# Optimization experiments

Hardware: AMD Instinct MI355X
Metric: run time of the kernel (lower is better)

The kernel has to match this reference:

```python
import jax, jax.numpy as jnp
import numpy as np

H = 300
V = 19495
B = 64
TU = 50
TT = 64


def gru(x, h0, Wih, Whh, bih, bhh, lens=None):
    """PyTorch-equation GRU, batch_first. x:[B,T,H], h0:[B,H].
    If lens is given, emulates pack/pad: outputs are zero past len,
    hidden state stops updating past len (final h = state at last valid step)."""
    Bx, T, _ = x.shape
    xg = jnp.einsum('bth,gh->btg', x, Wih) + bih          # [B,T,3H]
    xg = jnp.transpose(xg, (1, 0, 2))                      # [T,B,3H]
    if lens is None:
        mask = jnp.ones((T, Bx, 1), x.dtype)
    else:
        mask = (jnp.arange(T)[:, None] < lens[None, :]).astype(x.dtype)[..., None]  # [T,B,1]

    def step(h, tm):
        xg_t, m = tm
        hg = h @ Whh.T + bhh
        xr, xz, xn = jnp.split(xg_t, 3, axis=-1)
        hr, hz, hn = jnp.split(hg, 3, axis=-1)
        r = jax.nn.sigmoid(xr + hr)
        z = jax.nn.sigmoid(xz + hz)
        n = jnp.tanh(xn + r * hn)
        h_new = (1.0 - z) * n + z * h
        h = m * h_new + (1.0 - m) * h
        return h, h_new * m

    h_last, outs = jax.lax.scan(step, h0, (xg, mask))
    return jnp.transpose(outs, (1, 0, 2)), h_last


def setup_inputs() -> dict:
    key = jax.random.key(0)
    ks = jax.random.split(key, 24)
    s = 0.05
    p = {}
    p['emb_table'] = jax.random.normal(ks[0], (V, H), jnp.float32) * s
    for i, name in enumerate(['enc', 'sess', 'dec']):
        p[name + '_Wih'] = jax.random.normal(ks[1 + 4 * i], (3 * H, H), jnp.float32) * s
        p[name + '_Whh'] = jax.random.normal(ks[2 + 4 * i], (3 * H, H), jnp.float32) * s
        p[name + '_bih'] = jax.random.normal(ks[3 + 4 * i], (3 * H,), jnp.float32) * s
        p[name + '_bhh'] = jax.random.normal(ks[4 + 4 * i], (3 * H,), jnp.float32) * s
    p['out_W'] = jax.random.normal(ks[13], (V, H), jnp.float32) * s
    p['out_b'] = jax.random.normal(ks[14], (V,), jnp.float32) * s
    p['u1_input'] = jax.random.randint(ks[15], (B, TU), 0, V, jnp.int32)
    p['u1_lens'] = jax.random.randint(ks[16], (B,), 1, TU + 1, jnp.int32)
    p['u2_input'] = jax.random.randint(ks[17], (B, TU), 0, V, jnp.int32)
    p['u2_lens'] = jax.random.randint(ks[18], (B,), 1, TU + 1, jnp.int32)
    p['target_input'] = jax.random.randint(ks[19], (B, TT), 0, V, jnp.int32)
    p['target_input_lens'] = jax.random.randint(ks[20], (B,), 1, TT + 1, jnp.int32)
    return p


def reference(emb_table, enc_Wih, enc_Whh, enc_bih, enc_bhh,
              sess_Wih, sess_Whh, sess_bih, sess_bhh,
              dec_Wih, dec_Whh, dec_bih, dec_bhh,
              out_W, out_b,
              u1_input, u1_lens, u2_input, u2_lens,
              target_input, target_input_lens):
    h0 = jnp.zeros((B, H), jnp.float32)
    # utterance encoders (shared GRU), pack/pad semantics via masking
    _, u1_h = gru(emb_table[u1_input], h0, enc_Wih, enc_Whh, enc_bih, enc_bhh, u1_lens)
    _, u2_h = gru(emb_table[u2_input], h0, enc_Wih, enc_Whh, enc_bih, enc_bhh, u2_lens)
    si = jnp.stack([u1_h, u2_h], axis=1)  # [B,2,H]
    _, sess_h = gru(si, h0, sess_Wih, sess_Whh, sess_bih, sess_bhh)
    # teacher-forced decoder over all target steps
    tgt_emb = emb_table[target_input]      # [B,TT,H]
    dec_outs, _ = gru(tgt_emb, sess_h, dec_Wih, dec_Whh, dec_bih, dec_bhh)
    logits = jnp.einsum('bth,vh->btv', dec_outs, out_W) + out_b  # [B,TT,V]
    return logits
```

## Files before the change

### kernel.cpp

```cpp
#include <hip/hip_runtime.h>
#include <hip/hip_bf16.h>


#define HDIM 300
#define H3   900
#define KP   320
#define NV   19495
#define NVP  19584
#define NB   64
#define TUL  50
#define TTL  64

typedef short short8 __attribute__((ext_vector_type(8)));
typedef float f32x4  __attribute__((ext_vector_type(4)));

__device__ inline unsigned short f32_to_bf16(float f) {
  unsigned int u = __float_as_uint(f);
  u = u + 0x7FFFu + ((u >> 16) & 1u);
  return (unsigned short)(u >> 16);
}

__global__ void convert_pad_kernel(const float* __restrict__ src, short* __restrict__ dst, int rows) {
  int total = rows * HDIM;
  for (int i = blockIdx.x * blockDim.x + threadIdx.x; i < total; i += gridDim.x * blockDim.x) {
    int r = i / HDIM, c = i - r * HDIM;
    dst[(long)r * KP + c] = (short)f32_to_bf16(src[i]);
  }
}

__global__ void convert_A_kernel(const float* __restrict__ hdec, short* __restrict__ dst) {
  int total = TTL * HDIM * NB;
  for (int i = blockIdx.x * blockDim.x + threadIdx.x; i < total; i += gridDim.x * blockDim.x) {
    int t = i / (HDIM * NB);
    int rem = i - t * (HDIM * NB);
    int j = rem / NB;
    int b = rem - j * NB;
    dst[(long)(b * TTL + t) * KP + j] = (short)f32_to_bf16(hdec[i]);
  }
}

#define GM_PROJ 0
#define GM_XGE  1
#define GM_XGD  2

template <int MODE>
__launch_bounds__(256)
__global__ void mfma_gemm_kernel(const short* __restrict__ A,
                                 const short* __restrict__ B,
                                 const float* __restrict__ bias,
                                 float* __restrict__ C,
                                 const int* __restrict__ idx1,
                                 const int* __restrict__ idx2) {
  __shared__ short Asm[128 * 40];
  __shared__ short Bsm[128 * 40];
  int tid = threadIdx.x;
  int lane = tid & 63, wid = tid >> 6;
  int wm = wid >> 1, wn = wid & 1;
  int m0 = blockIdx.y * 128, n0 = blockIdx.x * 128;

  f32x4 acc[4][4] = {};

  int lrow = tid >> 2, lq = tid & 3;
  long arow[2], brow[2];
#pragma unroll
  for (int h = 0; h < 2; ++h) {
    int m = m0 + lrow + h * 64;
    long rowbase;
    if (MODE == GM_PROJ) {
      rowbase = (long)m * KP;
    } else if (MODE == GM_XGD) {
      rowbase = (long)idx1[m] * KP;
    } else {
      int u = m / 3200;
      int rm = m - u * 3200;
      int b = rm / TUL;
      int t = rm - b * TUL;
      int iv = u ? idx2[b * TUL + t] : idx1[b * TUL + t];
      rowbase = (long)iv * KP;
    }
    arow[h] = rowbase + lq * 8;
    brow[h] = (long)(n0 + lrow + h * 64) * KP + lq * 8;
  }

  for (int k0 = 0; k0 < KP; k0 += 32) {
#pragma unroll
    for (int h = 0; h < 2; ++h) {
      *(short8*)&Asm[(lrow + h * 64) * 40 + lq * 8] = *(const short8*)&A[arow[h] + k0];
      *(short8*)&Bsm[(lrow + h * 64) * 40 + lq * 8] = *(const short8*)&B[brow[h] + k0];
    }
    __syncthreads();
    int rlo = lane & 15, khi = (lane >> 4) * 8;
    short8 af[4], bfv[4];
#pragma unroll
    for (int i = 0; i < 4; ++i) af[i]  = *(const short8*)&Asm[(wm * 64 + i * 16 + rlo) * 40 + khi];
#pragma unroll
    for (int i = 0; i < 4; ++i) bfv[i] = *(const short8*)&Bsm[(wn * 64 + i * 16 + rlo) * 40 + khi];
#pragma unroll
    for (int i = 0; i < 4; ++i)
#pragma unroll
      for (int j = 0; j < 4; ++j)
        acc[i][j] = __builtin_amdgcn_mfma_f32_16x16x32_bf16(af[i], bfv[j], acc[i][j], 0, 0, 0);
    __syncthreads();
  }

  int rhi = (lane >> 4) * 4, cl = lane & 15;
#pragma unroll
  for (int i = 0; i < 4; ++i)
#pragma unroll
    for (int j = 0; j < 4; ++j) {
      int mb = m0 + wm * 64 + i * 16 + rhi;
      int n = n0 + wn * 64 + j * 16 + cl;
#pragma unroll
      for (int r = 0; r < 4; ++r) {
        int m = mb + r;
        float v = acc[i][j][r];
        if (MODE == GM_PROJ) {
          if (n < NV) C[(long)m * NV + n] = v + bias[n];
        } else if (MODE == GM_XGD) {
          if (n < H3) {
            int b = m >> 6, t = m & 63;
            C[(long)t * (H3 * NB) + n * NB + b] = v + bias[n];
          }
        } else {
          if (n < H3) {
            int u = m / 3200;
            int rm = m - u * 3200;
            int b = rm / TUL;
            int t = rm - b * TUL;
            C[(long)t * (H3 * 128) + n * 128 + u * 64 + b] = v + bias[n];
          }
        }
      }
    }
}

template <int BW, bool CX>
__launch_bounds__(256)
__global__ void gru_step_kernel(const float* __restrict__ Whh, const float* __restrict__ bhh,
                                const float* __restrict__ xg,
                                const float* __restrict__ Wih, const float* __restrict__ bih,
                                const float* __restrict__ x, int xstride,
                                const float* __restrict__ hin, float* __restrict__ hout,
                                const int* __restrict__ len1, const int* __restrict__ len2, int t) {
  int gt = blockIdx.x * blockDim.x + threadIdx.x;
  if (gt >= HDIM * BW) return;
  int col = gt & (BW - 1);
  int j = gt / BW;

  float hr = bhh[j], hz = bhh[HDIM + j], hn = bhh[2 * HDIM + j];
  const float* wr = Whh + (long)j * HDIM;
  const float* wz = Whh + (long)(HDIM + j) * HDIM;
  const float* wn = Whh + (long)(2 * HDIM + j) * HDIM;
  float xr = 0.f, xz = 0.f, xn = 0.f;
  const float* vr = nullptr;
  const float* vz = nullptr;
  const float* vn = nullptr;
  if (CX) {
    xr = bih[j]; xz = bih[HDIM + j]; xn = bih[2 * HDIM + j];
    vr = Wih + (long)j * HDIM;
    vz = Wih + (long)(HDIM + j) * HDIM;
    vn = Wih + (long)(2 * HDIM + j) * HDIM;
  }

#pragma unroll 4
  for (int k = 0; k < HDIM; ++k) {
    float hv = hin[k * BW + col];
    hr = fmaf(wr[k], hv, hr);
    hz = fmaf(wz[k], hv, hz);
    hn = fmaf(wn[k], hv, hn);
    if (CX) {
      float xv = x[k * xstride + col];
      xr = fmaf(vr[k], xv, xr);
      xz = fmaf(vz[k], xv, xz);
      xn = fmaf(vn[k], xv, xn);
    }
  }
  if (!CX) {
    xr = xg[j * BW + col];
    xz = xg[(HDIM + j) * BW + col];
    xn = xg[(2 * HDIM + j) * BW + col];
  }
  float r = 1.f / (1.f + __expf(-(xr + hr)));
  float z = 1.f / (1.f + __expf(-(xz + hz)));
  float n = tanhf(xn + r * hn);
  float hprev = hin[j * BW + col];
  float hnew = (1.f - z) * n + z * hprev;
  if (len1 != nullptr) {
    int L = (col < 64) ? len1[col] : len2[col - 64];
    if (t >= L) hnew = hprev;
  }
  hout[j * BW + col] = hnew;
}

extern "C" void kernel_launch(void* const* d_in, const int* in_sizes, int n_in,
                              void* d_out, int out_size, void* d_ws, size_t ws_size,
                              hipStream_t stream) {
  const float* emb      = (const float*)d_in[0];
  const float* enc_Wih  = (const float*)d_in[1];
  const float* enc_Whh  = (const float*)d_in[2];
  const float* enc_bih  = (const float*)d_in[3];
  const float* enc_bhh  = (const float*)d_in[4];
  const float* sess_Wih = (const float*)d_in[5];
  const float* sess_Whh = (const float*)d_in[6];
  const float* sess_bih = (const float*)d_in[7];
  const float* sess_bhh = (const float*)d_in[8];
  const float* dec_Wih  = (const float*)d_in[9];
  const float* dec_Whh  = (const float*)d_in[10];
  const float* dec_bih  = (const float*)d_in[11];
  const float* dec_bhh  = (const float*)d_in[12];
  const float* out_W    = (const float*)d_in[13];
  const float* out_b    = (const float*)d_in[14];
  const int* u1_in      = (const int*)d_in[15];
  const int* u1_lens    = (const int*)d_in[16];
  const int* u2_in      = (const int*)d_in[17];
  const int* u2_lens    = (const int*)d_in[18];
  const int* tgt_in     = (const int*)d_in[19];
  float* out = (float*)d_out;

  char* w = (char*)d_ws;
  auto alloc = [&](size_t bytes) -> char* {
    char* p = w;
    w += (bytes + 255) & ~(size_t)255;
    return p;
  };
  short* emb_bf  = (short*)alloc((size_t)NV  * KP * 2);
  short* wie_bf  = (short*)alloc((size_t)1024 * KP * 2);
  short* wid_bf  = (short*)alloc((size_t)1024 * KP * 2);
  short* wout_bf = (short*)alloc((size_t)NVP * KP * 2);
  short* a_bf    = (short*)alloc((size_t)4096 * KP * 2);
  char* bf_end = w;
  float* h_enc0 = (float*)alloc((size_t)HDIM * 128 * 4);
  float* h_enc1 = (float*)alloc((size_t)HDIM * 128 * 4);
  float* h_s0   = (float*)alloc((size_t)HDIM * NB * 4);
  float* h_s1   = (float*)alloc((size_t)HDIM * NB * 4);
  char* h_end = w;
  float* xg_enc = (float*)alloc((size_t)TUL * H3 * 128 * 4);
  float* xg_dec = (float*)alloc((size_t)TTL * H3 * NB * 4);
  float* h_dec  = (float*)alloc((size_t)TTL * HDIM * NB * 4);

  hipMemsetAsync(emb_bf, 0, (size_t)(bf_end - (char*)emb_bf), stream);
  hipMemsetAsync(h_enc0, 0, (size_t)(h_end - (char*)h_enc0), stream);

  convert_pad_kernel<<<1024, 256, 0, stream>>>(emb, emb_bf, NV);
  convert_pad_kernel<<<64, 256, 0, stream>>>(enc_Wih, wie_bf, H3);
  convert_pad_kernel<<<64, 256, 0, stream>>>(dec_Wih, wid_bf, H3);
  convert_pad_kernel<<<1024, 256, 0, stream>>>(out_W, wout_bf, NV);

  {
    dim3 g(8, 50);
    mfma_gemm_kernel<GM_XGE><<<g, 256, 0, stream>>>(emb_bf, wie_bf, enc_bih, xg_enc, u1_in, u2_in);
  }
  {
    dim3 g(8, 32);
    mfma_gemm_kernel<GM_XGD><<<g, 256, 0, stream>>>(emb_bf, wid_bf, dec_bih, xg_dec, tgt_in, nullptr);
  }

  float* hb[2] = {h_enc0, h_enc1};
  for (int t = 0; t < TUL; ++t) {
    gru_step_kernel<128, false><<<150, 256, 0, stream>>>(
        enc_Whh, enc_bhh, xg_enc + (long)t * H3 * 128,
        nullptr, nullptr, nullptr, 0,
        hb[t & 1], hb[(t + 1) & 1], u1_lens, u2_lens, t);
  }
  float* encf = hb[0];

  float* sb[2] = {h_s0, h_s1};
  for (int t = 0; t < 2; ++t) {
    gru_step_kernel<64, true><<<75, 256, 0, stream>>>(
        sess_Whh, sess_bhh, nullptr,
        sess_Wih, sess_bih, encf + t * 64, 128,
        sb[t & 1], sb[(t + 1) & 1], nullptr, nullptr, t);
  }
  float* sessf = sb[0];

  for (int t = 0; t < TTL; ++t) {
    const float* hin = (t == 0) ? sessf : (h_dec + (long)(t - 1) * HDIM * NB);
    gru_step_kernel<64, false><<<75, 256, 0, stream>>>(
        dec_Whh, dec_bhh, xg_dec + (long)t * H3 * NB,
        nullptr, nullptr, nullptr, 0,
        hin, h_dec + (long)t * HDIM * NB, nullptr, nullptr, t);
  }

  convert_A_kernel<<<512, 256, 0, stream>>>(h_dec, a_bf);
  {
    dim3 g(153, 32);
    mfma_gemm_kernel<GM_PROJ><<<g, 256, 0, stream>>>(a_bf, wout_bf, out_b, out, nullptr, nullptr);
  }
}
```

Before: 3.518 ms.

## Fuse all GRU recurrences into one persistent MFMA kernel per batch slice

Replaces the 116 per-timestep fp32 GRU step launches and the separate conversion kernel with a single persistent kernel of 8 blocks. Each block owns 8 batch rows and keeps its hidden state in shared memory across the encoder, session and decoder phases. The recurrent matvecs run as bf16 MFMA, and the bf16 decoder outputs are written straight into the projection A matrix. This removes launch overhead and the global round trips of hidden state, but uses only 8 CUs and re-reads the recurrent weights from L2 every step. Rounding the recurrent weights and state to bf16 adds precision risk.

```diff
diff --git a/kernel.cpp b/kernel.cpp
--- a/kernel.cpp
+++ b/kernel.cpp
@@ -10,6 +10,8 @@
 #define NB   64
 #define TUL  50
 #define TTL  64
+#define HS   328
+#define HFS  301
 
 typedef short short8 __attribute__((ext_vector_type(8)));
 typedef float f32x4  __attribute__((ext_vector_type(4)));
@@ -25,17 +27,6 @@
   for (int i = blockIdx.x * blockDim.x + threadIdx.x; i < total; i += gridDim.x * blockDim.x) {
     int r = i / HDIM, c = i - r * HDIM;
     dst[(long)r * KP + c] = (short)f32_to_bf16(src[i]);
-  }
-}
-
-__global__ void convert_A_kernel(const float* __restrict__ hdec, short* __restrict__ dst) {
-  int total = TTL * HDIM * NB;
-  for (int i = blockIdx.x * blockDim.x + threadIdx.x; i < total; i += gridDim.x * blockDim.x) {
-    int t = i / (HDIM * NB);
-    int rem = i - t * (HDIM * NB);
-    int j = rem / NB;
-    int b = rem - j * NB;
-    dst[(long)(b * TTL + t) * KP + j] = (short)f32_to_bf16(hdec[i]);
   }
 }
 
@@ -134,62 +125,160 @@
     }
 }
 
-template <int BW, bool CX>
-__launch_bounds__(256)
-__global__ void gru_step_kernel(const float* __restrict__ Whh, const float* __restrict__ bhh,
-                                const float* __restrict__ xg,
-                                const float* __restrict__ Wih, const float* __restrict__ bih,
-                                const float* __restrict__ x, int xstride,
-                                const float* __restrict__ hin, float* __restrict__ hout,
-                                const int* __restrict__ len1, const int* __restrict__ len2, int t) {
-  int gt = blockIdx.x * blockDim.x + threadIdx.x;
-  if (gt >= HDIM * BW) return;
-  int col = gt & (BW - 1);
-  int j = gt / BW;
-
-  float hr = bhh[j], hz = bhh[HDIM + j], hn = bhh[2 * HDIM + j];
-  const float* wr = Whh + (long)j * HDIM;
-  const float* wz = Whh + (long)(HDIM + j) * HDIM;
-  const float* wn = Whh + (long)(2 * HDIM + j) * HDIM;
-  float xr = 0.f, xz = 0.f, xn = 0.f;
-  const float* vr = nullptr;
-  const float* vz = nullptr;
-  const float* vn = nullptr;
-  if (CX) {
-    xr = bih[j]; xz = bih[HDIM + j]; xn = bih[2 * HDIM + j];
-    vr = Wih + (long)j * HDIM;
-    vz = Wih + (long)(HDIM + j) * HDIM;
-    vn = Wih + (long)(2 * HDIM + j) * HDIM;
-  }
-
-#pragma unroll 4
-  for (int k = 0; k < HDIM; ++k) {
-    float hv = hin[k * BW + col];
-    hr = fmaf(wr[k], hv, hr);
-    hz = fmaf(wz[k], hv, hz);
-    hn = fmaf(wn[k], hv, hn);
-    if (CX) {
-      float xv = x[k * xstride + col];
-      xr = fmaf(vr[k], xv, xr);
-      xz = fmaf(vz[k], xv, xz);
-      xn = fmaf(vn[k], xv, xn);
-    }
-  }
-  if (!CX) {
-    xr = xg[j * BW + col];
-    xz = xg[(HDIM + j) * BW + col];
-    xn = xg[(2 * HDIM + j) * BW + col];
-  }
-  float r = 1.f / (1.f + __expf(-(xr + hr)));
-  float z = 1.f / (1.f + __expf(-(xz + hz)));
-  float n = tanhf(xn + r * hn);
-  float hprev = hin[j * BW + col];
-  float hnew = (1.f - z) * n + z * hprev;
-  if (len1 != nullptr) {
-    int L = (col < 64) ? len1[col] : len2[col - 64];
-    if (t >= L) hnew = hprev;
-  }
-  hout[j * BW + col] = hnew;
+__device__ __forceinline__ void run_chunks(const short* __restrict__ Wb,
+                                           const short8 (&af)[10],
+                                           f32x4 (&acc)[5][3],
+                                           int wv, int lane) {
+  int jc = lane & 15;
+  int kh = (lane >> 4) * 8;
+  short8 bb[3][10];
+  auto issue = [&](int c, short8 (&buf)[10]) {
+    int tw = c / 3, g = c - tw * 3;
+    const short* p = Wb + (long)(g * HDIM + (wv + 4 * tw) * 16 + jc) * KP + kh;
+#pragma unroll
+    for (int kk = 0; kk < 10; ++kk) buf[kk] = *(const short8*)(p + kk * 32);
+  };
+  issue(0, bb[0]);
+  issue(1, bb[1]);
+#pragma unroll
+  for (int c = 0; c < 15; ++c) {
+    if (c + 2 < 15) issue(c + 2, bb[(c + 2) % 3]);
+    int tw = c / 3, g = c - tw * 3;
+#pragma unroll
+    for (int kk = 0; kk < 10; ++kk)
+      acc[tw][g] = __builtin_amdgcn_mfma_f32_16x16x32_bf16(af[kk], bb[c % 3][kk], acc[tw][g], 0, 0, 0);
+  }
+}
+
+template <int MODE>
+__device__ __forceinline__ void gru_fused_step(
+    int w, int wv, int lane, int t,
+    const short* __restrict__ Wb, const float* __restrict__ xg,
+    float* __restrict__ hF, short* __restrict__ hbf,
+    const float* __restrict__ bhhL, const float* __restrict__ xgS,
+    const int* __restrict__ lensL, short* __restrict__ abf) {
+  int jc = lane & 15, kh = (lane >> 4) * 8, mh = lane >> 4;
+  short8 af[10];
+#pragma unroll
+  for (int kk = 0; kk < 10; ++kk)
+    af[kk] = *(const short8*)&hbf[jc * HS + kk * 32 + kh];
+  __syncthreads();
+  f32x4 acc[5][3];
+#pragma unroll
+  for (int a = 0; a < 5; ++a)
+#pragma unroll
+    for (int g = 0; g < 3; ++g) acc[a][g] = (f32x4){0.f, 0.f, 0.f, 0.f};
+  run_chunks(Wb, af, acc, wv, lane);
+#pragma unroll
+  for (int tw = 0; tw < 5; ++tw) {
+    int jm = (wv + 4 * tw) * 16 + jc;
+    bool jok = jm < HDIM;
+    int j = jok ? jm : 0;
+    float br = bhhL[j], bz = bhhL[HDIM + j], bn = bhhL[2 * HDIM + j];
+#pragma unroll
+    for (int r = 0; r < 4; ++r) {
+      int m = mh * 4 + r;
+      float XR, XZ, XN;
+      if (MODE == 0) {
+        int col = (m < 8) ? (8 * w + m) : (64 + 8 * w + (m - 8));
+        const float* b = xg + ((long)t * H3 + j) * 128 + col;
+        XR = b[0]; XZ = b[HDIM * 128]; XN = b[2 * HDIM * 128];
+      } else if (MODE == 1) {
+        int col = 8 * w + (m & 7);
+        const float* b = xg + ((long)t * H3 + j) * NB + col;
+        XR = b[0]; XZ = b[HDIM * NB]; XN = b[2 * HDIM * NB];
+      } else {
+        XR = xgS[(0 * KP + j) * 17 + m];
+        XZ = xgS[(1 * KP + j) * 17 + m];
+        XN = xgS[(2 * KP + j) * 17 + m];
+      }
+      float HRv = acc[tw][0][r] + br;
+      float HZv = acc[tw][1][r] + bz;
+      float HNv = acc[tw][2][r] + bn;
+      float rg = 1.f / (1.f + __expf(-(XR + HRv)));
+      float zg = 1.f / (1.f + __expf(-(XZ + HZv)));
+      float ng = tanhf(XN + rg * HNv);
+      float hp = hF[m * HFS + j];
+      float hnew = (1.f - zg) * ng + zg * hp;
+      if (MODE == 0 && t >= lensL[m]) hnew = hp;
+      bool mok = (MODE == 0) || (m < 8);
+      if (jok && mok) {
+        hF[m * HFS + jm] = hnew;
+        short hb = (short)f32_to_bf16(hnew);
+        hbf[m * HS + jm] = hb;
+        if (MODE == 1) abf[((long)(8 * w + m) * TTL + t) * KP + jm] = hb;
+      }
+    }
+  }
+  __syncthreads();
+}
+
+__launch_bounds__(256, 1)
+__global__ void fused_recurrence_kernel(
+    const short* __restrict__ WhhE, const short* __restrict__ WhhSs,
+    const short* __restrict__ WihSs, const short* __restrict__ WhhD,
+    const float* __restrict__ bhhE_g, const float* __restrict__ bhhS_g,
+    const float* __restrict__ bihS_g, const float* __restrict__ bhhD_g,
+    const float* __restrict__ xgE, const float* __restrict__ xgD,
+    const int* __restrict__ u1l, const int* __restrict__ u2l,
+    short* __restrict__ abf) {
+  __shared__ float hF1[16 * HFS];
+  __shared__ short hb1[16 * HS];
+  __shared__ float hF2[16 * HFS];
+  __shared__ short hb2[16 * HS];
+  __shared__ float xgS[3 * KP * 17];
+  __shared__ float bhhL[H3];
+  __shared__ int lensL[16];
+  int tid = threadIdx.x, lane = tid & 63, wv = tid >> 6, w = blockIdx.x;
+
+  for (int i = tid; i < 16 * HFS; i += 256) { hF1[i] = 0.f; hF2[i] = 0.f; }
+  for (int i = tid; i < 16 * HS; i += 256) { hb1[i] = 0; hb2[i] = 0; }
+  if (tid < 8) lensL[tid] = u1l[8 * w + tid];
+  else if (tid < 16) lensL[tid] = u2l[8 * w + tid - 8];
+  for (int i = tid; i < H3; i += 256) bhhL[i] = bhhE_g[i];
+  __syncthreads();
+
+  for (int t = 0; t < TUL; ++t)
+    gru_fused_step<0>(w, wv, lane, t, WhhE, xgE, hF1, hb1, bhhL, nullptr, lensL, nullptr);
+
+  for (int i = tid; i < H3; i += 256) bhhL[i] = bhhS_g[i];
+  __syncthreads();
+  for (int t = 0; t < 2; ++t) {
+    {
+      int jc = lane & 15, kh = (lane >> 4) * 8, mh = lane >> 4;
+      int xrow = 8 * t + (jc & 7);
+      short8 af[10];
+#pragma unroll
+      for (int kk = 0; kk < 10; ++kk)
+        af[kk] = *(const short8*)&hb1[xrow * HS + kk * 32 + kh];
+      f32x4 acc[5][3];
+#pragma unroll
+      for (int a = 0; a < 5; ++a)
+#pragma unroll
+        for (int g = 0; g < 3; ++g) acc[a][g] = (f32x4){0.f, 0.f, 0.f, 0.f};
+      run_chunks(WihSs, af, acc, wv, lane);
+#pragma unroll
+      for (int tw = 0; tw < 5; ++tw) {
+        int jm = (wv + 4 * tw) * 16 + jc;
+        if (jm < HDIM) {
+#pragma unroll
+          for (int g = 0; g < 3; ++g) {
+            float bi = bihS_g[g * HDIM + jm];
+#pragma unroll
+            for (int r = 0; r < 4; ++r)
+              xgS[(g * KP + jm) * 17 + (mh * 4 + r)] = acc[tw][g][r] + bi;
+          }
+        }
+      }
+      __syncthreads();
+    }
+    gru_fused_step<2>(w, wv, lane, t, WhhSs, nullptr, hF2, hb2, bhhL, xgS, nullptr, nullptr);
+  }
+
+  for (int i = tid; i < H3; i += 256) bhhL[i] = bhhD_g[i];
+  __syncthreads();
+  for (int t = 0; t < TTL; ++t)
+    gru_fused_step<1>(w, wv, lane, t, WhhD, xgD, hF2, hb2, bhhL, nullptr, nullptr, abf);
 }
 
 extern "C" void kernel_launch(void* const* d_in, const int* in_sizes, int n_in,
@@ -228,23 +317,24 @@
   short* wid_bf  = (short*)alloc((size_t)1024 * KP * 2);
   short* wout_bf = (short*)alloc((size_t)NVP * KP * 2);
   short* a_bf    = (short*)alloc((size_t)4096 * KP * 2);
+  short* whhE_bf = (short*)alloc((size_t)960 * KP * 2);
+  short* whhS_bf = (short*)alloc((size_t)960 * KP * 2);
+  short* wihS_bf = (short*)alloc((size_t)960 * KP * 2);
+  short* whhD_bf = (short*)alloc((size_t)960 * KP * 2);
   char* bf_end = w;
-  float* h_enc0 = (float*)alloc((size_t)HDIM * 128 * 4);
-  float* h_enc1 = (float*)alloc((size_t)HDIM * 128 * 4);
-  float* h_s0   = (float*)alloc((size_t)HDIM * NB * 4);
-  float* h_s1   = (float*)alloc((size_t)HDIM * NB * 4);
-  char* h_end = w;
   float* xg_enc = (float*)alloc((size_t)TUL * H3 * 128 * 4);
   float* xg_dec = (float*)alloc((size_t)TTL * H3 * NB * 4);
-  float* h_dec  = (float*)alloc((size_t)TTL * HDIM * NB * 4);
 
   hipMemsetAsync(emb_bf, 0, (size_t)(bf_end - (char*)emb_bf), stream);
-  hipMemsetAsync(h_enc0, 0, (size_t)(h_end - (char*)h_enc0), stream);
 
   convert_pad_kernel<<<1024, 256, 0, stream>>>(emb, emb_bf, NV);
   convert_pad_kernel<<<64, 256, 0, stream>>>(enc_Wih, wie_bf, H3);
   convert_pad_kernel<<<64, 256, 0, stream>>>(dec_Wih, wid_bf, H3);
   convert_pad_kernel<<<1024, 256, 0, stream>>>(out_W, wout_bf, NV);
+  convert_pad_kernel<<<64, 256, 0, stream>>>(enc_Whh, whhE_bf, H3);
+  convert_pad_kernel<<<64, 256, 0, stream>>>(sess_Whh, whhS_bf, H3);
+  convert_pad_kernel<<<64, 256, 0, stream>>>(sess_Wih, wihS_bf, H3);
+  convert_pad_kernel<<<64, 256, 0, stream>>>(dec_Whh, whhD_bf, H3);
 
   {
     dim3 g(8, 50);
@@ -255,33 +345,11 @@
     mfma_gemm_kernel<GM_XGD><<<g, 256, 0, stream>>>(emb_bf, wid_bf, dec_bih, xg_dec, tgt_in, nullptr);
   }
 
-  float* hb[2] = {h_enc0, h_enc1};
-  for (int t = 0; t < TUL; ++t) {
-    gru_step_kernel<128, false><<<150, 256, 0, stream>>>(
-        enc_Whh, enc_bhh, xg_enc + (long)t * H3 * 128,
-        nullptr, nullptr, nullptr, 0,
-        hb[t & 1], hb[(t + 1) & 1], u1_lens, u2_lens, t);
-  }
-  float* encf = hb[0];
-
-  float* sb[2] = {h_s0, h_s1};
-  for (int t = 0; t < 2; ++t) {
-    gru_step_kernel<64, true><<<75, 256, 0, stream>>>(
-        sess_Whh, sess_bhh, nullptr,
-        sess_Wih, sess_bih, encf + t * 64, 128,
-        sb[t & 1], sb[(t + 1) & 1], nullptr, nullptr, t);
-  }
-  float* sessf = sb[0];
-
-  for (int t = 0; t < TTL; ++t) {
-    const float* hin = (t == 0) ? sessf : (h_dec + (long)(t - 1) * HDIM * NB);
-    gru_step_kernel<64, false><<<75, 256, 0, stream>>>(
-        dec_Whh, dec_bhh, xg_dec + (long)t * H3 * NB,
-        nullptr, nullptr, nullptr, 0,
-        hin, h_dec + (long)t * HDIM * NB, nullptr, nullptr, t);
-  }
-
-  convert_A_kernel<<<512, 256, 0, stream>>>(h_dec, a_bf);
+  fused_recurrence_kernel<<<8, 256, 0, stream>>>(
+      whhE_bf, whhS_bf, wihS_bf, whhD_bf,
+      enc_bhh, sess_bhh, sess_bih, dec_bhh,
+      xg_enc, xg_dec, u1_lens, u2_lens, a_bf);
+
   {
     dim3 g(153, 32);
     mfma_gemm_kernel<GM_PROJ><<<g, 256, 0, stream>>>(a_bf, wout_bf, out_b, out, nullptr, nullptr);
```

After: 3.029 ms. 1.16x faster.
